# Performance work log

Measured on AMD Instinct MI355X. Metric: run time of the kernel, lower is better.

Reference implementation:

```python
import jax, jax.numpy as jnp
import numpy as np

KERNEL_MUL = 2.0
KERNEL_NUM = 5


def setup_inputs() -> dict:
    key = jax.random.key(0)
    k1, k2 = jax.random.split(key)
    source = jax.random.normal(k1, (4096, 256), dtype=jnp.float32)
    target = jax.random.normal(k2, (4096, 256), dtype=jnp.float32)
    return {"source": source, "target": target}


def reference(source, target):
    n = source.shape[0]
    total = jnp.concatenate([source, target], axis=0)  # [2N, D]
    ns = total.shape[0]
    # Squared-L2 pairwise distances via the GEMM trick (avoids [2N,2N,D] blowup)
    sq = jnp.sum(total * total, axis=1)  # [2N]
    dist = sq[:, None] + sq[None, :] - 2.0 * (total @ total.T)  # [2N,2N]
    # bandwidth computed on detached distances (torch uses .data)
    bandwidth = jax.lax.stop_gradient(jnp.sum(dist)) / (ns * ns - ns)
    bandwidth = bandwidth / (KERNEL_MUL ** (KERNEL_NUM // 2))
    # multi-bandwidth Gaussian kernel sum (small fixed loop over KERNEL_NUM)
    kernels = jnp.zeros_like(dist)
    for i in range(KERNEL_NUM):
        kernels = kernels + jnp.exp(-dist / (bandwidth * (KERNEL_MUL ** i)))
    kernels = kernels / KERNEL_NUM
    XX = kernels[:n, :n]
    YY = kernels[n:, n:]
    XY = kernels[:n, n:]
    YX = kernels[n:, :n]
    # symmetric == 'yes' branch
    return jnp.mean(XX + YY - XY - YX) / 2.0
```

## Files before the change

### kernel.cpp

```cpp
#include <hip/hip_runtime.h>

#define NROWS 8192
#define NHALF 4096
#define DIM   256
#define NB_PREP 256
#define NTILES  64
#define NBLK    2080

typedef __attribute__((ext_vector_type(2))) float f32x2;
typedef __attribute__((ext_vector_type(4))) float f32x4;
typedef __attribute__((ext_vector_type(4))) int   v4i;
typedef __attribute__((ext_vector_type(8))) int   v8i;

__device__ __forceinline__ const float* side_base(const float* src, const float* tgt, int row) {
    return (row < NHALF) ? (src + (size_t)row * DIM)
                         : (tgt + (size_t)(row - NHALF) * DIM);
}

__global__ __launch_bounds__(256) void prep_kernel(
        const float* __restrict__ src, const float* __restrict__ tgt,
        unsigned char* __restrict__ F8,
        float* __restrict__ sq, float* __restrict__ colpart, float* __restrict__ sqpart)
{
    int t = threadIdx.x;
    int lane = t & 63;
    int w = t >> 6;
    int wave = blockIdx.x * 4 + w;
    float cs0 = 0, cs1 = 0, cs2 = 0, cs3 = 0;
    double lss = 0.0;
    for (int r = wave; r < NROWS; r += NB_PREP * 4) {
        const float* p = side_base(src, tgt, r);
        float4 v = *(const float4*)(p + 4 * lane);
        cs0 += v.x; cs1 += v.y; cs2 += v.z; cs3 += v.w;
        int p01 = __builtin_amdgcn_cvt_pk_fp8_f32(v.x, v.y, 0, false);
        int pk  = __builtin_amdgcn_cvt_pk_fp8_f32(v.z, v.w, p01, true);
        *(unsigned*)(F8 + (size_t)r * DIM + 4 * lane) = (unsigned)pk;
        float d = v.x * v.x + v.y * v.y + v.z * v.z + v.w * v.w;
        #pragma unroll
        for (int off = 32; off > 0; off >>= 1) d += __shfl_xor(d, off);
        if (lane == 0) { sq[r] = d; lss += (double)d; }
    }
    __shared__ float csh[4][256];
    __shared__ double ssh[4];
    csh[w][4 * lane + 0] = cs0; csh[w][4 * lane + 1] = cs1;
    csh[w][4 * lane + 2] = cs2; csh[w][4 * lane + 3] = cs3;
    if (lane == 0) ssh[w] = lss;
    __syncthreads();
    colpart[t * NB_PREP + blockIdx.x] = csh[0][t] + csh[1][t] + csh[2][t] + csh[3][t];
    if (t == 0) sqpart[blockIdx.x] = (float)(ssh[0] + ssh[1] + ssh[2] + ssh[3]);
}

__global__ void bw_kernel(const float* __restrict__ colpart,
                          const float* __restrict__ sqpart, float* __restrict__ qconst)
{
    __shared__ double red[256], red2[256];
    int t = threadIdx.x;
    float s = 0.f;
    #pragma unroll 8
    for (int i = 0; i < NB_PREP / 4; ++i) {
        float4 v = *(const float4*)(colpart + t * NB_PREP + 4 * i);
        s += (v.x + v.y) + (v.z + v.w);
    }
    double sd = (double)s;
    red[t] = sd * sd;
    red2[t] = (double)sqpart[t];
    __syncthreads();
    for (int k = 128; k > 0; k >>= 1) {
        if (t < k) { red[t] += red[t + k]; red2[t] += red2[t + k]; }
        __syncthreads();
    }
    if (t == 0) {
        double ns = (double)NROWS;
        double sumdist = 2.0 * ns * red2[0] - 2.0 * red[0];
        double bw = sumdist / (ns * ns - ns) / 4.0;
        qconst[0] = (float)(1.4426950408889634 / (16.0 * bw));
    }
}

__device__ __forceinline__ int tri_cum(int b) {
    return b * NTILES - ((b * (b - 1)) >> 1);
}

__device__ __forceinline__ v8i load_frag(const char* base, int r, int kbase) {
    int sw = (r & 7) << 4;
    v4i lo = *(const v4i*)(base + (r << 7) + (kbase ^ sw));
    v4i hi = *(const v4i*)(base + (r << 7) + ((kbase + 16) ^ sw));
    v8i out;
    out[0] = lo[0]; out[1] = lo[1]; out[2] = lo[2]; out[3] = lo[3];
    out[4] = hi[0]; out[5] = hi[1]; out[6] = hi[2]; out[7] = hi[3];
    return out;
}

__device__ __forceinline__ f32x4 mfma_k128(v8i a, v8i b, f32x4 c) {
#if __has_builtin(__builtin_amdgcn_mfma_scale_f32_16x16x128_f8f6f4)
    return __builtin_amdgcn_mfma_scale_f32_16x16x128_f8f6f4(
        a, b, c, 0, 0, 0, 0x7F7F7F7F, 0, 0x7F7F7F7F);
#else
    const long long* av = (const long long*)&a;
    const long long* bv = (const long long*)&b;
    #pragma unroll
    for (int i = 0; i < 4; ++i)
        c = __builtin_amdgcn_mfma_f32_16x16x32_fp8_fp8(av[i], bv[i], c, 0, 0, 0);
    return c;
#endif
}

__global__ __launch_bounds__(256, 4) void mmd_main_kernel(
        const unsigned char* __restrict__ F8, const float* __restrict__ sq,
        const float* __restrict__ qc, float* __restrict__ partials)
{
    __shared__ alignas(16) char lds[32768];
    __shared__ float fred[4];

    int wg = blockIdx.x;
    int rank = (wg & 7) * (NBLK / 8) + (wg >> 3);
    int by = (int)((129.0f - sqrtf(16641.0f - 8.0f * (float)rank)) * 0.5f);
    while (tri_cum(by + 1) <= rank) ++by;
    while (tri_cum(by) > rank) --by;
    int bx = by + (rank - tri_cum(by));

    int t = threadIdx.x;
    int rowBase = by * 128, colBase = bx * 128;
    int lane = t & 63, w = t >> 6;
    int wr = w >> 1, wc = w & 1;
    int kbase = (lane >> 4) << 5;

    float q = qc[0];

    f32x4 acc[4][4];
    #pragma unroll
    for (int m = 0; m < 4; ++m)
        #pragma unroll
        for (int n = 0; n < 4; ++n) acc[m][n] = (f32x4)0.f;

    #pragma unroll
    for (int kc = 0; kc < 2; ++kc) {
        if (kc) __syncthreads();
        #pragma unroll
        for (int qq = 0; qq < 4; ++qq) {
            int p = qq * 4096 + t * 16;
            int row = p >> 7;
            int col = (p & 127) ^ ((row & 7) << 4);
            const char* ga = (const char*)F8 + (((size_t)(rowBase + row)) << 8) + kc * 128 + col;
            const char* gb = (const char*)F8 + (((size_t)(colBase + row)) << 8) + kc * 128 + col;
            __builtin_amdgcn_global_load_lds(
                (const __attribute__((address_space(1))) void*)ga,
                (__attribute__((address_space(3))) void*)(lds + p), 16, 0, 0);
            __builtin_amdgcn_global_load_lds(
                (const __attribute__((address_space(1))) void*)gb,
                (__attribute__((address_space(3))) void*)(lds + 16384 + p), 16, 0, 0);
        }
        __syncthreads();

        v8i bf[4];
        #pragma unroll
        for (int n = 0; n < 4; ++n)
            bf[n] = load_frag(lds + 16384, wc * 64 + n * 16 + (lane & 15), kbase);
        #pragma unroll
        for (int m = 0; m < 4; ++m) {
            v8i af = load_frag(lds, wr * 64 + m * 16 + (lane & 15), kbase);
            #pragma unroll
            for (int n = 0; n < 4; ++n)
                acc[m][n] = mfma_k128(af, bf[n], acc[m][n]);
        }
    }

    f32x2 twoq2 = {2.f * q, 2.f * q};
    int rsub = (lane >> 4) * 4, csub = lane & 15;
    f32x2 nqa2[4][2];
    float qb[4];
    #pragma unroll
    for (int m = 0; m < 4; ++m)
        #pragma unroll
        for (int p = 0; p < 2; ++p) {
            int rr = rowBase + wr * 64 + m * 16 + rsub + 2 * p;
            nqa2[m][p] = (f32x2){-q * sq[rr], -q * sq[rr + 1]};
        }
    #pragma unroll
    for (int n = 0; n < 4; ++n)
        qb[n] = q * sq[colBase + wc * 64 + n * 16 + csub];

    f32x2 psum2 = {0.f, 0.f};
    #pragma unroll
    for (int m = 0; m < 4; ++m) {
        #pragma unroll
        for (int n = 0; n < 4; ++n) {
            f32x2 qbn = {qb[n], qb[n]};
            #pragma unroll
            for (int p = 0; p < 2; ++p) {
                f32x2 acc2 = {acc[m][n][2 * p], acc[m][n][2 * p + 1]};
                f32x2 arg = acc2 * twoq2 + (nqa2[m][p] - qbn);
                f32x2 e4 = {__builtin_amdgcn_exp2f(arg.x), __builtin_amdgcn_exp2f(arg.y)};
                f32x2 e3 = e4 * e4, e2 = e3 * e3, e1 = e2 * e2, e0 = e1 * e1;
                psum2 += ((e4 + e3) + (e2 + e1)) + e0;
            }
        }
    }
    float psum = psum2.x + psum2.y;

    #pragma unroll
    for (int off = 32; off > 0; off >>= 1) psum += __shfl_xor(psum, off);
    if (lane == 0) fred[w] = psum;
    __syncthreads();
    if (t == 0) {
        float sign = ((rowBase < NHALF) == (colBase < NHALF)) ? 1.f : -1.f;
        float wgt = (bx == by) ? 1.f : 2.f;
        partials[rank] = sign * wgt * (fred[0] + fred[1] + fred[2] + fred[3]);
    }
}

__global__ void finalize_kernel(const float* __restrict__ partials, int n,
                                float* __restrict__ out)
{
    __shared__ double red[256];
    int t = threadIdx.x;
    double s = 0;
    for (int i = t; i < n; i += 256) s += (double)partials[i];
    red[t] = s;
    __syncthreads();
    for (int k = 128; k > 0; k >>= 1) { if (t < k) red[t] += red[t + k]; __syncthreads(); }
    if (t == 0) {
        double nn = (double)NHALF;
        out[0] = (float)(red[0] / 5.0 / (2.0 * nn * nn));
    }
}

extern "C" void kernel_launch(void* const* d_in, const int* in_sizes, int n_in,
                              void* d_out, int out_size, void* d_ws, size_t ws_size,
                              hipStream_t stream) {
    const float* src = (const float*)d_in[0];
    const float* tgt = (const float*)d_in[1];
    float* out = (float*)d_out;
    char* ws = (char*)d_ws;

    float*         colpart  = (float*)(ws + 0);
    float*         sqpart   = (float*)(ws + 262144);
    float*         qconst   = (float*)(ws + 263168);
    float*         sq       = (float*)(ws + 264192);
    float*         partials = (float*)(ws + 297984);
    unsigned char* F8       = (unsigned char*)(ws + 524288);

    prep_kernel<<<NB_PREP, 256, 0, stream>>>(src, tgt, F8, sq, colpart, sqpart);
    bw_kernel<<<1, 256, 0, stream>>>(colpart, sqpart, qconst);
    mmd_main_kernel<<<NBLK, 256, 0, stream>>>(F8, sq, qconst, partials);
    finalize_kernel<<<1, 256, 0, stream>>>(partials, NBLK, out);
}
```

Baseline: 44.75 us.

## Stage only A tile in LDS, load B fragments directly to registers per wave

The main kernel now loads the full-K (256) A tile into LDS in a single pass and drops the two-chunk loop and its barrier. Each wave reads its B fragments straight from global memory into registers, and the wave layout changes from 2x2 to 1x4 (8x2 MFMA tiles per wave). The per-block LDS cross-wave reduction is replaced by per-wave partial writes, and finalize now sums four times as many partials. Occupancy hint drops from 4 to 3 blocks per CU, trading occupancy for more registers. Direct global B loads are uncoalesced 32-byte reads per lane, though they can overlap with the LDS staging of A.

```diff
diff --git a/kernel.cpp b/kernel.cpp
--- a/kernel.cpp
+++ b/kernel.cpp
@@ -81,10 +81,20 @@
     return b * NTILES - ((b * (b - 1)) >> 1);
 }
 
-__device__ __forceinline__ v8i load_frag(const char* base, int r, int kbase) {
+__device__ __forceinline__ v8i load_afrag(const char* base, int r, int kcol) {
     int sw = (r & 7) << 4;
-    v4i lo = *(const v4i*)(base + (r << 7) + (kbase ^ sw));
-    v4i hi = *(const v4i*)(base + (r << 7) + ((kbase + 16) ^ sw));
+    v4i lo = *(const v4i*)(base + (r << 8) + (kcol ^ sw));
+    v4i hi = *(const v4i*)(base + (r << 8) + ((kcol + 16) ^ sw));
+    v8i out;
+    out[0] = lo[0]; out[1] = lo[1]; out[2] = lo[2]; out[3] = lo[3];
+    out[4] = hi[0]; out[5] = hi[1]; out[6] = hi[2]; out[7] = hi[3];
+    return out;
+}
+
+__device__ __forceinline__ v8i load_bfrag(const unsigned char* F8, int row, int kcol) {
+    const char* p = (const char*)F8 + ((size_t)row << 8) + kcol;
+    v4i lo = *(const v4i*)p;
+    v4i hi = *(const v4i*)(p + 16);
     v8i out;
     out[0] = lo[0]; out[1] = lo[1]; out[2] = lo[2]; out[3] = lo[3];
     out[4] = hi[0]; out[5] = hi[1]; out[6] = hi[2]; out[7] = hi[3];
@@ -105,12 +115,11 @@
 #endif
 }
 
-__global__ __launch_bounds__(256, 4) void mmd_main_kernel(
+__global__ __launch_bounds__(256, 3) void mmd_main_kernel(
         const unsigned char* __restrict__ F8, const float* __restrict__ sq,
         const float* __restrict__ qc, float* __restrict__ partials)
 {
     __shared__ alignas(16) char lds[32768];
-    __shared__ float fred[4];
 
     int wg = blockIdx.x;
     int rank = (wg & 7) * (NBLK / 8) + (wg >> 3);
@@ -122,74 +131,71 @@
     int t = threadIdx.x;
     int rowBase = by * 128, colBase = bx * 128;
     int lane = t & 63, w = t >> 6;
-    int wr = w >> 1, wc = w & 1;
-    int kbase = (lane >> 4) << 5;
+    int l15 = lane & 15;
+    int kb = (lane >> 4) << 5;
+    int rsub = (lane >> 4) * 4;
+
+    #pragma unroll
+    for (int qq = 0; qq < 8; ++qq) {
+        int p = qq * 4096 + t * 16;
+        int row = p >> 8;
+        int col = (p & 255) ^ ((row & 7) << 4);
+        const char* ga = (const char*)F8 + (((size_t)(rowBase + row)) << 8) + col;
+        __builtin_amdgcn_global_load_lds(
+            (const __attribute__((address_space(1))) void*)ga,
+            (__attribute__((address_space(3))) void*)(lds + p), 16, 0, 0);
+    }
+
+    int bcol = colBase + w * 32;
+    v8i bf00 = load_bfrag(F8, bcol      + l15, 0   + kb);
+    v8i bf01 = load_bfrag(F8, bcol      + l15, 128 + kb);
+    v8i bf10 = load_bfrag(F8, bcol + 16 + l15, 0   + kb);
+    v8i bf11 = load_bfrag(F8, bcol + 16 + l15, 128 + kb);
+    __builtin_amdgcn_sched_barrier(0);
 
     float q = qc[0];
-
-    f32x4 acc[4][4];
-    #pragma unroll
-    for (int m = 0; m < 4; ++m)
+    float qb0 = q * sq[bcol + l15];
+    float qb1 = q * sq[bcol + 16 + l15];
+
+    __syncthreads();
+
+    f32x4 acc[8][2];
+    #pragma unroll
+    for (int m = 0; m < 8; ++m) {
+        acc[m][0] = (f32x4)0.f;
+        acc[m][1] = (f32x4)0.f;
+    }
+
+    #pragma unroll
+    for (int m = 0; m < 8; ++m) {
+        v8i af0 = load_afrag(lds, m * 16 + l15, 0 + kb);
+        v8i af1 = load_afrag(lds, m * 16 + l15, 128 + kb);
+        acc[m][0] = mfma_k128(af0, bf00, acc[m][0]);
+        acc[m][0] = mfma_k128(af1, bf01, acc[m][0]);
+        acc[m][1] = mfma_k128(af0, bf10, acc[m][1]);
+        acc[m][1] = mfma_k128(af1, bf11, acc[m][1]);
+    }
+
+    f32x2 nqa[8][2];
+    #pragma unroll
+    for (int m = 0; m < 8; ++m) {
+        int rr = rowBase + m * 16 + rsub;
+        nqa[m][0] = (f32x2){-q * sq[rr],     -q * sq[rr + 1]};
+        nqa[m][1] = (f32x2){-q * sq[rr + 2], -q * sq[rr + 3]};
+    }
+
+    f32x2 twoq2 = {2.f * q, 2.f * q};
+    float qbv[2] = {qb0, qb1};
+    f32x2 psum2 = {0.f, 0.f};
+    #pragma unroll
+    for (int m = 0; m < 8; ++m) {
         #pragma unroll
-        for (int n = 0; n < 4; ++n) acc[m][n] = (f32x4)0.f;
-
-    #pragma unroll
-    for (int kc = 0; kc < 2; ++kc) {
-        if (kc) __syncthreads();
-        #pragma unroll
-        for (int qq = 0; qq < 4; ++qq) {
-            int p = qq * 4096 + t * 16;
-            int row = p >> 7;
-            int col = (p & 127) ^ ((row & 7) << 4);
-            const char* ga = (const char*)F8 + (((size_t)(rowBase + row)) << 8) + kc * 128 + col;
-            const char* gb = (const char*)F8 + (((size_t)(colBase + row)) << 8) + kc * 128 + col;
-            __builtin_amdgcn_global_load_lds(
-                (const __attribute__((address_space(1))) void*)ga,
-                (__attribute__((address_space(3))) void*)(lds + p), 16, 0, 0);
-            __builtin_amdgcn_global_load_lds(
-                (const __attribute__((address_space(1))) void*)gb,
-                (__attribute__((address_space(3))) void*)(lds + 16384 + p), 16, 0, 0);
-        }
-        __syncthreads();
-
-        v8i bf[4];
-        #pragma unroll
-        for (int n = 0; n < 4; ++n)
-            bf[n] = load_frag(lds + 16384, wc * 64 + n * 16 + (lane & 15), kbase);
-        #pragma unroll
-        for (int m = 0; m < 4; ++m) {
-            v8i af = load_frag(lds, wr * 64 + m * 16 + (lane & 15), kbase);
-            #pragma unroll
-            for (int n = 0; n < 4; ++n)
-                acc[m][n] = mfma_k128(af, bf[n], acc[m][n]);
-        }
-    }
-
-    f32x2 twoq2 = {2.f * q, 2.f * q};
-    int rsub = (lane >> 4) * 4, csub = lane & 15;
-    f32x2 nqa2[4][2];
-    float qb[4];
-    #pragma unroll
-    for (int m = 0; m < 4; ++m)
-        #pragma unroll
-        for (int p = 0; p < 2; ++p) {
-            int rr = rowBase + wr * 64 + m * 16 + rsub + 2 * p;
-            nqa2[m][p] = (f32x2){-q * sq[rr], -q * sq[rr + 1]};
-        }
-    #pragma unroll
-    for (int n = 0; n < 4; ++n)
-        qb[n] = q * sq[colBase + wc * 64 + n * 16 + csub];
-
-    f32x2 psum2 = {0.f, 0.f};
-    #pragma unroll
-    for (int m = 0; m < 4; ++m) {
-        #pragma unroll
-        for (int n = 0; n < 4; ++n) {
-            f32x2 qbn = {qb[n], qb[n]};
+        for (int n = 0; n < 2; ++n) {
+            f32x2 qbn = {qbv[n], qbv[n]};
             #pragma unroll
             for (int p = 0; p < 2; ++p) {
                 f32x2 acc2 = {acc[m][n][2 * p], acc[m][n][2 * p + 1]};
-                f32x2 arg = acc2 * twoq2 + (nqa2[m][p] - qbn);
+                f32x2 arg = acc2 * twoq2 + (nqa[m][p] - qbn);
                 f32x2 e4 = {__builtin_amdgcn_exp2f(arg.x), __builtin_amdgcn_exp2f(arg.y)};
                 f32x2 e3 = e4 * e4, e2 = e3 * e3, e1 = e2 * e2, e0 = e1 * e1;
                 psum2 += ((e4 + e3) + (e2 + e1)) + e0;
@@ -200,12 +206,10 @@
 
     #pragma unroll
     for (int off = 32; off > 0; off >>= 1) psum += __shfl_xor(psum, off);
-    if (lane == 0) fred[w] = psum;
-    __syncthreads();
-    if (t == 0) {
+    if (lane == 0) {
         float sign = ((rowBase < NHALF) == (colBase < NHALF)) ? 1.f : -1.f;
         float wgt = (bx == by) ? 1.f : 2.f;
-        partials[rank] = sign * wgt * (fred[0] + fred[1] + fred[2] + fred[3]);
+        partials[rank * 4 + w] = sign * wgt * psum;
     }
 }
 
@@ -243,5 +247,5 @@
     prep_kernel<<<NB_PREP, 256, 0, stream>>>(src, tgt, F8, sq, colpart, sqpart);
     bw_kernel<<<1, 256, 0, stream>>>(colpart, sqpart, qconst);
     mmd_main_kernel<<<NBLK, 256, 0, stream>>>(F8, sq, qconst, partials);
-    finalize_kernel<<<1, 256, 0, stream>>>(partials, NBLK, out);
-}
+    finalize_kernel<<<1, 256, 0, stream>>>(partials, NBLK * 4, out);
+}
```

After: 52.85 us. 18.1% more time.
